# Kernel optimization log

Measured on AMD Instinct MI355X. Metric: run time of the kernel, lower is better.

The kernel has to match this reference:

```python
import jax, jax.numpy as jnp
import numpy as np

B, S, D = 2, 4096, 1024
H = 16            # num_attention_heads
HD = D // H       # head_dim = 64
WIN = 256         # sliding_window_size
STEP = WIN // 2   # loop stride in the original torch code
NB = S // STEP    # number of query blocks of size STEP
EPS = 1e-5


def setup_inputs() -> dict:
    key = jax.random.key(0)
    ks = jax.random.split(key, 6)
    lin = lambda k: jax.random.normal(k, (D, D), jnp.float32) * 0.02
    return {
        "hidden_states": jax.random.normal(ks[0], (B, S, D), jnp.float32),
        "Wq": lin(ks[1]), "bq": jnp.zeros((D,), jnp.float32),
        "Wk": lin(ks[2]), "bk": jnp.zeros((D,), jnp.float32),
        "Wv": lin(ks[3]), "bv": jnp.zeros((D,), jnp.float32),
        "Wo": lin(ks[4]), "bo": jnp.zeros((D,), jnp.float32),
        "ln_w": jnp.ones((D,), jnp.float32),
        "ln_b": jnp.zeros((D,), jnp.float32),
    }


def _split_heads(x):
    # [B,S,D] -> [B,H,S,HD]
    b, s, _ = x.shape
    return x.reshape(b, s, H, HD).transpose(0, 2, 1, 3)


def _forward(hidden_states, Wq, bq, Wk, bk, Wv, bv, Wo, bo, ln_w, ln_b):
    q = _split_heads(hidden_states @ Wq + bq)
    k = _split_heads(hidden_states @ Wk + bk)
    v = _split_heads(hidden_states @ Wv + bv)

    # windows overwrite earlier ones. Net effect: query block i (rows
    qb = q.reshape(B, H, NB, STEP, HD)
    kb = k.reshape(B, H, NB, STEP, HD)
    vb = v.reshape(B, H, NB, STEP, HD)
    zpad = jnp.zeros_like(kb[:, :, :1])
    k_win = jnp.concatenate([kb, jnp.concatenate([kb[:, :, 1:], zpad], axis=2)], axis=3)
    v_win = jnp.concatenate([vb, jnp.concatenate([vb[:, :, 1:], zpad], axis=2)], axis=3)

    scores = jnp.einsum("bhnqd,bhnkd->bhnqk", qb, k_win) / jnp.sqrt(jnp.float32(HD))
    # last block has only STEP valid keys (window truncated at seq end)
    blk = jnp.arange(NB)[:, None]
    kpos = jnp.arange(WIN)[None, :]
    valid = (blk < NB - 1) | (kpos < STEP)
    scores = jnp.where(valid[None, None, :, None, :], scores, -jnp.inf)
    attn = jax.nn.softmax(scores, axis=-1)
    outb = jnp.einsum("bhnqk,bhnkd->bhnqd", attn, v_win)  # [B,H,NB,STEP,HD]

    attn_out = outb.reshape(B, H, S, HD).transpose(0, 2, 1, 3).reshape(B, S, D)
    attn_out = attn_out @ Wo + bo

    x = hidden_states + attn_out
    mu = jnp.mean(x, axis=-1, keepdims=True)
    var = jnp.mean(jnp.square(x - mu), axis=-1, keepdims=True)
    return (x - mu) * jax.lax.rsqrt(var + EPS) * ln_w + ln_b


def reference(hidden_states, Wq, bq, Wk, bk, Wv, bv, Wo, bo, ln_w, ln_b):
    return _forward(hidden_states, Wq, bq, Wk, bk, Wv, bv, Wo, bo, ln_w, ln_b)
```

## Files before the change

kernel.cpp:

```cpp
#include <hip/hip_runtime.h>
#include <hip/hip_bf16.h>
#include <stdint.h>

#define D_MODEL 1024
#define SEQ     4096
#define NHEADS  16
#define HEAD_DIM 64
#define NBLK    32
#define MROWS   8192

typedef unsigned short u16;
using bf16x8 = __attribute__((ext_vector_type(8))) short;
using f32x4  = __attribute__((ext_vector_type(4))) float;

__device__ __forceinline__ float b2f(u16 b) {
  union { unsigned int u; float f; } v; v.u = ((unsigned int)b) << 16; return v.f;
}
__device__ __forceinline__ u16 f2b(float f) {
  union { float f; unsigned int u; } v; v.f = f;
  return (u16)((v.u + 0x7FFFu + ((v.u >> 16) & 1u)) >> 16);
}

__device__ __forceinline__ void gload16(const u16* g, u16* l) {
  __builtin_amdgcn_global_load_lds((const __attribute__((address_space(1))) void*)g,
                                   (__attribute__((address_space(3))) void*)l, 16, 0, 0);
}

__global__ __launch_bounds__(256) void convert_x_kernel(const float* __restrict__ X,
                                                        u16* __restrict__ Xb) {
  size_t idx = (size_t)blockIdx.x * 2048 + (size_t)threadIdx.x * 8;
  float4 a = *(const float4*)(X + idx);
  float4 b = *(const float4*)(X + idx + 4);
  union { u16 u[8]; uint4 v; } o;
  o.u[0]=f2b(a.x); o.u[1]=f2b(a.y); o.u[2]=f2b(a.z); o.u[3]=f2b(a.w);
  o.u[4]=f2b(b.x); o.u[5]=f2b(b.y); o.u[6]=f2b(b.z); o.u[7]=f2b(b.w);
  *(uint4*)(Xb + idx) = o.v;
}

__global__ __launch_bounds__(256) void transpose_w_kernel(const float* __restrict__ Wq,
                                                          const float* __restrict__ Wk,
                                                          const float* __restrict__ Wv,
                                                          const float* __restrict__ Wo,
                                                          u16* __restrict__ Wt) {
  const float* W = (blockIdx.z == 0) ? Wq : (blockIdx.z == 1) ? Wk
                 : (blockIdx.z == 2) ? Wv : Wo;
  u16* out = Wt + (size_t)blockIdx.z * D_MODEL * D_MODEL;
  __shared__ float t[32][33];
  int x = blockIdx.x * 32;
  int y = blockIdx.y * 32;
  int tx = threadIdx.x & 31, ty = threadIdx.x >> 5;
#pragma unroll
  for (int p = 0; p < 4; ++p)
    t[ty + p * 8][tx] = W[(size_t)(y + ty + p * 8) * D_MODEL + x + tx];
  __syncthreads();
#pragma unroll
  for (int p = 0; p < 4; ++p)
    out[(size_t)(x + ty + p * 8) * D_MODEL + y + tx] = f2b(t[tx][ty + p * 8]);
}

__device__ __forceinline__ void gemm_core(const u16* __restrict__ Ag,
                                          const u16* __restrict__ Bg,
                                          int m0, int n0,
                                          u16* smem, f32x4 acc[4][4]) {
  const int tid  = threadIdx.x;
  const int lane = tid & 63;
  const int w    = tid >> 6;
  const int wm   = w >> 1, wn = w & 1;
  const int fr   = lane & 15;

#pragma unroll
  for (int mf = 0; mf < 4; ++mf)
#pragma unroll
    for (int nf = 0; nf < 4; ++nf)
      acc[mf][nf] = (f32x4)(0.0f);

  const int srow = w * 32 + (lane >> 3);
  const int scol = (lane & 7) * 8;
  const u16* agp = Ag + (size_t)(m0 + srow) * D_MODEL + scol;
  const u16* bgp = Bg + (size_t)(n0 + srow) * D_MODEL + scol;
  u16* asl = smem + w * 2048;
  u16* bsl = smem + 8192 + w * 2048;

  const u16* ars = smem + (wm * 64 + fr) * 64 + (lane >> 4) * 8;
  const u16* brs = smem + 8192 + (wn * 64 + fr) * 64 + (lane >> 4) * 8;

  for (int kt = 0; kt < D_MODEL / 64; ++kt) {
#pragma unroll
    for (int j = 0; j < 4; ++j) {
      gload16(agp + (size_t)(j * 8) * D_MODEL, asl + j * 512);
      gload16(bgp + (size_t)(j * 8) * D_MODEL, bsl + j * 512);
    }
    agp += 64; bgp += 64;
    __syncthreads();
#pragma unroll
    for (int kk = 0; kk < 2; ++kk) {
      bf16x8 a[4], b[4];
#pragma unroll
      for (int mf = 0; mf < 4; ++mf)
        a[mf] = *(const bf16x8*)(ars + mf * 1024 + kk * 32);
#pragma unroll
      for (int nf = 0; nf < 4; ++nf)
        b[nf] = *(const bf16x8*)(brs + nf * 1024 + kk * 32);
#pragma unroll
      for (int mf = 0; mf < 4; ++mf)
#pragma unroll
        for (int nf = 0; nf < 4; ++nf)
          acc[mf][nf] = __builtin_amdgcn_mfma_f32_16x16x32_bf16(a[mf], b[nf],
                                                                acc[mf][nf], 0, 0, 0);
    }
    __syncthreads();
  }
}

__global__ __launch_bounds__(256, 2) void qkv_gemm_kernel(const u16* __restrict__ Xb,
                                                          const u16* __restrict__ Wt,
                                                          const float* __restrict__ bq,
                                                          const float* __restrict__ bk,
                                                          const float* __restrict__ bv,
                                                          u16* __restrict__ Qb,
                                                          u16* __restrict__ Kb,
                                                          u16* __restrict__ Vt) {
  __shared__ u16 smem[16384];
  const int id  = blockIdx.x;
  const int lin = (id & 7) * 192 + (id >> 3);
  const int which = lin % 3;
  const int nr  = lin / 3;
  const int n0  = (nr & 7) * 128;
  const int m0  = (nr >> 3) * 128;
  const u16* Bg = Wt + (size_t)which * D_MODEL * D_MODEL;
  f32x4 acc[4][4];
  gemm_core(Xb, Bg, m0, n0, smem, acc);

  const float* bias = (which == 0) ? bq : (which == 1) ? bk : bv;
  const float scale = (which == 0) ? 0.125f : 1.0f;
  const int lane = threadIdx.x & 63, w = threadIdx.x >> 6;
  const int wm = w >> 1, wn = w & 1;
  const int fr = lane & 15, fg = lane >> 4;
  const int mb = wm * 64 + fg * 4;
  const int nb = wn * 64 + fr;

  if (which < 2) {
#pragma unroll
    for (int nf = 0; nf < 4; ++nf) {
      const int n = nb + nf * 16;
      const float bn = bias[n0 + n];
#pragma unroll
      for (int mf = 0; mf < 4; ++mf)
#pragma unroll
        for (int r = 0; r < 4; ++r)
          smem[(mb + mf * 16 + r) * 128 + n] = f2b((acc[mf][nf][r] + bn) * scale);
    }
  } else {
#pragma unroll
    for (int nf = 0; nf < 4; ++nf) {
      const int n = nb + nf * 16;
      const float bn = bias[n0 + n];
#pragma unroll
      for (int mf = 0; mf < 4; ++mf)
#pragma unroll
        for (int r = 0; r < 4; ++r)
          smem[n * 128 + mb + mf * 16 + r] = f2b(acc[mf][nf][r] + bn);
    }
  }
  __syncthreads();

  u16* outQK = (which == 0) ? Qb : Kb;
#pragma unroll
  for (int it = 0; it < 2; ++it) {
    const int c   = threadIdx.x + it * 256;
    const int row = c >> 2;
    const int o32 = (c & 3) * 32;
    const u16* src = smem + row * 128 + o32;
    uint4 v0 = *(const uint4*)(src);
    uint4 v1 = *(const uint4*)(src + 8);
    uint4 v2 = *(const uint4*)(src + 16);
    uint4 v3 = *(const uint4*)(src + 24);
    u16* dst;
    if (which < 2) {
      const int mg = m0 + row;
      const int bb = mg >> 12, s = mg & 4095;
      const int n  = n0 + o32;
      const int h  = n >> 6, d0 = n & 63;
      dst = outQK + ((size_t)(bb * NHEADS + h) * SEQ + s) * HEAD_DIM + d0;
    } else {
      const int n  = n0 + row;
      const int h  = n >> 6, d = n & 63;
      const int bb = m0 >> 12;
      dst = Vt + ((size_t)(bb * NHEADS + h) * HEAD_DIM + d) * SEQ + (m0 & 4095) + o32;
    }
    *(uint4*)dst = v0; *(uint4*)(dst + 8) = v1;
    *(uint4*)(dst + 16) = v2; *(uint4*)(dst + 24) = v3;
  }
}

__global__ __launch_bounds__(256, 2) void o_gemm_kernel(const u16* __restrict__ X2,
                                                        const u16* __restrict__ WtO,
                                                        const float* __restrict__ bo,
                                                        u16* __restrict__ Y) {
  __shared__ u16 smem[16384];
  const int id  = blockIdx.x;
  const int lin = (id & 7) * 64 + (id >> 3);
  const int n0  = (lin & 7) * 128;
  const int m0  = (lin >> 3) * 128;
  f32x4 acc[4][4];
  gemm_core(X2, WtO, m0, n0, smem, acc);

  const int lane = threadIdx.x & 63, w = threadIdx.x >> 6;
  const int wm = w >> 1, wn = w & 1;
  const int fr = lane & 15, fg = lane >> 4;
  const int mb = wm * 64 + fg * 4;
  const int nb = wn * 64 + fr;
#pragma unroll
  for (int nf = 0; nf < 4; ++nf) {
    const int n = nb + nf * 16;
    const float bn = bo[n0 + n];
#pragma unroll
    for (int mf = 0; mf < 4; ++mf)
#pragma unroll
      for (int r = 0; r < 4; ++r)
        smem[(mb + mf * 16 + r) * 128 + n] = f2b(acc[mf][nf][r] + bn);
  }
  __syncthreads();
#pragma unroll
  for (int it = 0; it < 2; ++it) {
    const int c   = threadIdx.x + it * 256;
    const int row = c >> 2;
    const int o32 = (c & 3) * 32;
    const u16* src = smem + row * 128 + o32;
    uint4 v0 = *(const uint4*)(src);
    uint4 v1 = *(const uint4*)(src + 8);
    uint4 v2 = *(const uint4*)(src + 16);
    uint4 v3 = *(const uint4*)(src + 24);
    u16* dst = Y + (size_t)(m0 + row) * D_MODEL + n0 + o32;
    *(uint4*)dst = v0; *(uint4*)(dst + 8) = v1;
    *(uint4*)(dst + 16) = v2; *(uint4*)(dst + 24) = v3;
  }
}

#define PSTR 264
#define OSTR 72

template <int NF>
__device__ __forceinline__ void attn_body(const u16* __restrict__ Qp,
                                          const u16* __restrict__ Kp,
                                          const u16* __restrict__ Vp,
                                          u16* __restrict__ X2p,
                                          u16* Ps, float* rs) {
  const int lane = threadIdx.x & 63;
  const int fr = lane & 15, fg = lane >> 4;

  bf16x8 qf[2][2];
#pragma unroll
  for (int mf = 0; mf < 2; ++mf)
#pragma unroll
    for (int kk = 0; kk < 2; ++kk)
      qf[mf][kk] = *(const bf16x8*)(Qp + (mf * 16 + fr) * HEAD_DIM + kk * 32 + fg * 8);

  f32x4 sacc[2][NF];
#pragma unroll
  for (int mf = 0; mf < 2; ++mf)
#pragma unroll
    for (int nf = 0; nf < NF; ++nf) sacc[mf][nf] = (f32x4)(0.0f);

#pragma unroll
  for (int nf = 0; nf < NF; ++nf) {
    bf16x8 kf0 = *(const bf16x8*)(Kp + (nf * 16 + fr) * HEAD_DIM + fg * 8);
    bf16x8 kf1 = *(const bf16x8*)(Kp + (nf * 16 + fr) * HEAD_DIM + 32 + fg * 8);
#pragma unroll
    for (int mf = 0; mf < 2; ++mf) {
      sacc[mf][nf] = __builtin_amdgcn_mfma_f32_16x16x32_bf16(qf[mf][0], kf0, sacc[mf][nf], 0, 0, 0);
      sacc[mf][nf] = __builtin_amdgcn_mfma_f32_16x16x32_bf16(qf[mf][1], kf1, sacc[mf][nf], 0, 0, 0);
    }
  }

#pragma unroll
  for (int mf = 0; mf < 2; ++mf) {
#pragma unroll
    for (int r = 0; r < 4; ++r) {
      float mx = -1e30f;
#pragma unroll
      for (int nf = 0; nf < NF; ++nf) mx = fmaxf(mx, sacc[mf][nf][r]);
      mx = fmaxf(mx, __shfl_xor(mx, 1));
      mx = fmaxf(mx, __shfl_xor(mx, 2));
      mx = fmaxf(mx, __shfl_xor(mx, 4));
      mx = fmaxf(mx, __shfl_xor(mx, 8));
      float sm = 0.f;
#pragma unroll
      for (int nf = 0; nf < NF; ++nf) {
        float p = __expf(sacc[mf][nf][r] - mx);
        sacc[mf][nf][r] = p;
        sm += p;
      }
      sm += __shfl_xor(sm, 1);
      sm += __shfl_xor(sm, 2);
      sm += __shfl_xor(sm, 4);
      sm += __shfl_xor(sm, 8);
      if (fr == 0) rs[mf * 16 + fg * 4 + r] = sm;
    }
  }

#pragma unroll
  for (int mf = 0; mf < 2; ++mf)
#pragma unroll
    for (int nf = 0; nf < NF; ++nf)
#pragma unroll
      for (int r = 0; r < 4; ++r)
        Ps[(mf * 16 + fg * 4 + r) * PSTR + nf * 16 + fr] = f2b(sacc[mf][nf][r]);
  __syncthreads();

  f32x4 oacc[4][2];
#pragma unroll
  for (int mf2 = 0; mf2 < 4; ++mf2)
#pragma unroll
    for (int nf2 = 0; nf2 < 2; ++nf2) oacc[mf2][nf2] = (f32x4)(0.0f);

#pragma unroll
  for (int ks = 0; ks < NF / 2; ++ks) {
    bf16x8 vf[4];
#pragma unroll
    for (int mf2 = 0; mf2 < 4; ++mf2)
      vf[mf2] = *(const bf16x8*)(Vp + (size_t)(mf2 * 16 + fr) * SEQ + ks * 32 + fg * 8);
#pragma unroll
    for (int nf2 = 0; nf2 < 2; ++nf2) {
      bf16x8 pf = *(const bf16x8*)(Ps + (nf2 * 16 + fr) * PSTR + ks * 32 + fg * 8);
#pragma unroll
      for (int mf2 = 0; mf2 < 4; ++mf2)
        oacc[mf2][nf2] = __builtin_amdgcn_mfma_f32_16x16x32_bf16(vf[mf2], pf,
                                                                 oacc[mf2][nf2], 0, 0, 0);
    }
  }
  __syncthreads();

#pragma unroll
  for (int nf2 = 0; nf2 < 2; ++nf2) {
    const int q = nf2 * 16 + fr;
    const float inv = 1.0f / rs[q];
#pragma unroll
    for (int mf2 = 0; mf2 < 4; ++mf2)
#pragma unroll
      for (int r = 0; r < 4; ++r)
        Ps[q * OSTR + mf2 * 16 + fg * 4 + r] = f2b(oacc[mf2][nf2][r] * inv);
  }
  __syncthreads();
  const int q2 = lane >> 1, hf = (lane & 1) * 32;
  const u16* osrc = Ps + q2 * OSTR + hf;
  uint4 o0 = *(const uint4*)(osrc);
  uint4 o1 = *(const uint4*)(osrc + 8);
  uint4 o2 = *(const uint4*)(osrc + 16);
  uint4 o3 = *(const uint4*)(osrc + 24);
  u16* dst = X2p + (size_t)q2 * D_MODEL + hf;
  *(uint4*)dst = o0; *(uint4*)(dst + 8) = o1;
  *(uint4*)(dst + 16) = o2; *(uint4*)(dst + 24) = o3;
}

__global__ __launch_bounds__(256, 2) void attn_kernel(const u16* __restrict__ Qb,
                                                      const u16* __restrict__ Kb,
                                                      const u16* __restrict__ Vt,
                                                      u16* __restrict__ X2) {
  __shared__ u16 Ps[4][32 * PSTR];
  __shared__ float rs[4][32];
  const int bx = blockIdx.x;
  const int bh = bx >> 5, i = bx & 31;
  const int w = threadIdx.x >> 6;
  const int b = bh >> 4, h = bh & 15;
  const u16* Qp = Qb + ((size_t)bh * SEQ + i * 128 + w * 32) * HEAD_DIM;
  const u16* Kp = Kb + ((size_t)bh * SEQ + i * 128) * HEAD_DIM;
  const u16* Vp = Vt + (size_t)bh * HEAD_DIM * SEQ + i * 128;
  u16* X2p = X2 + ((size_t)(b * SEQ) + i * 128 + w * 32) * D_MODEL + h * HEAD_DIM;
  if (i == NBLK - 1) attn_body<8>(Qp, Kp, Vp, X2p, Ps[w], rs[w]);
  else               attn_body<16>(Qp, Kp, Vp, X2p, Ps[w], rs[w]);
}

__global__ __launch_bounds__(256) void ln_kernel(const float* __restrict__ hidden,
                                                 const u16* __restrict__ Y,
                                                 const float* __restrict__ lw,
                                                 const float* __restrict__ lb,
                                                 float* __restrict__ out) {
  const int row = blockIdx.x;
  const int tid = threadIdx.x;
  const size_t base = (size_t)row * D_MODEL + tid * 4;
  float4 h = *(const float4*)(hidden + base);
  union { uint2 v; u16 u[4]; } y;
  y.v = *(const uint2*)(Y + base);
  float x0 = h.x + b2f(y.u[0]);
  float x1 = h.y + b2f(y.u[1]);
  float x2 = h.z + b2f(y.u[2]);
  float x3 = h.w + b2f(y.u[3]);
  float sum = x0 + x1 + x2 + x3;
  float sq  = x0 * x0 + x1 * x1 + x2 * x2 + x3 * x3;
#pragma unroll
  for (int off = 32; off >= 1; off >>= 1) {
    sum += __shfl_down(sum, off);
    sq  += __shfl_down(sq, off);
  }
  __shared__ float s1[4], s2[4];
  const int w = tid >> 6, lane = tid & 63;
  if (lane == 0) { s1[w] = sum; s2[w] = sq; }
  __syncthreads();
  const float ts = s1[0] + s1[1] + s1[2] + s1[3];
  const float tq = s2[0] + s2[1] + s2[2] + s2[3];
  const float mu = ts * (1.0f / 1024.0f);
  const float var = tq * (1.0f / 1024.0f) - mu * mu;
  const float rstd = rsqrtf(var + 1e-5f);
  float4 lwv = *(const float4*)(lw + tid * 4);
  float4 lbv = *(const float4*)(lb + tid * 4);
  float4 o;
  o.x = (x0 - mu) * rstd * lwv.x + lbv.x;
  o.y = (x1 - mu) * rstd * lwv.y + lbv.y;
  o.z = (x2 - mu) * rstd * lwv.z + lbv.z;
  o.w = (x3 - mu) * rstd * lwv.w + lbv.w;
  *(float4*)(out + base) = o;
}

extern "C" void kernel_launch(void* const* d_in, const int* in_sizes, int n_in,
                              void* d_out, int out_size, void* d_ws, size_t ws_size,
                              hipStream_t stream) {
  const float* hidden = (const float*)d_in[0];
  const float* Wq = (const float*)d_in[1];
  const float* bq = (const float*)d_in[2];
  const float* Wk = (const float*)d_in[3];
  const float* bk = (const float*)d_in[4];
  const float* Wv = (const float*)d_in[5];
  const float* bv = (const float*)d_in[6];
  const float* Wo = (const float*)d_in[7];
  const float* bo = (const float*)d_in[8];
  const float* lw = (const float*)d_in[9];
  const float* lb = (const float*)d_in[10];
  float* out = (float*)d_out;

  u16* Xb = (u16*)d_ws;
  u16* Wt = Xb + (size_t)MROWS * D_MODEL;
  u16* Qb = Wt + (size_t)4 * D_MODEL * D_MODEL;
  u16* Kb = Qb + (size_t)32 * SEQ * HEAD_DIM;
  u16* Vt = Kb + (size_t)32 * SEQ * HEAD_DIM;
  u16* X2 = Vt + (size_t)32 * SEQ * HEAD_DIM;
  u16* Y  = X2 + (size_t)MROWS * D_MODEL;

  convert_x_kernel<<<4096, 256, 0, stream>>>(hidden, Xb);
  transpose_w_kernel<<<dim3(32, 32, 4), 256, 0, stream>>>(Wq, Wk, Wv, Wo, Wt);
  qkv_gemm_kernel<<<1536, 256, 0, stream>>>(Xb, Wt, bq, bk, bv, Qb, Kb, Vt);
  attn_kernel<<<1024, 256, 0, stream>>>(Qb, Kb, Vt, X2);
  o_gemm_kernel<<<512, 256, 0, stream>>>(X2, Wt + (size_t)3 * D_MODEL * D_MODEL, bo, Y);
  ln_kernel<<<MROWS, 256, 0, stream>>>(hidden, Y, lw, lb, out);
}
```

Baseline: 268.3 us.

## Double-buffer GEMM LDS tiles with prefetch and XOR-swizzled layout

The shared GEMM core now keeps two LDS buffers and issues the global-to-LDS loads for the next K tile before computing on the current one, waiting with a partial vmcnt so load latency overlaps the MFMA work. It also XOR-swizzles the 16-byte chunk placement in LDS to reduce bank conflicts on fragment reads. LDS per block doubles to 64 KB, which may limit how many blocks fit per CU at the requested occupancy of 2.

New measurement: 258.1 us. 3.8% less time.

```diff
diff --git a/kernel.cpp b/kernel.cpp
--- a/kernel.cpp
+++ b/kernel.cpp
@@ -8,6 +8,7 @@
 #define HEAD_DIM 64
 #define NBLK    32
 #define MROWS   8192
+#define NKT     16
 
 typedef unsigned short u16;
 using bf16x8 = __attribute__((ext_vector_type(8))) short;
@@ -67,6 +68,7 @@
   const int w    = tid >> 6;
   const int wm   = w >> 1, wn = w & 1;
   const int fr   = lane & 15;
+  const int fg   = lane >> 4;
 
 #pragma unroll
   for (int mf = 0; mf < 4; ++mf)
@@ -74,41 +76,64 @@
     for (int nf = 0; nf < 4; ++nf)
       acc[mf][nf] = (f32x4)(0.0f);
 
-  const int srow = w * 32 + (lane >> 3);
-  const int scol = (lane & 7) * 8;
-  const u16* agp = Ag + (size_t)(m0 + srow) * D_MODEL + scol;
-  const u16* bgp = Bg + (size_t)(n0 + srow) * D_MODEL + scol;
-  u16* asl = smem + w * 2048;
-  u16* bsl = smem + 8192 + w * 2048;
-
-  const u16* ars = smem + (wm * 64 + fr) * 64 + (lane >> 4) * 8;
-  const u16* brs = smem + 8192 + (wn * 64 + fr) * 64 + (lane >> 4) * 8;
-
-  for (int kt = 0; kt < D_MODEL / 64; ++kt) {
+  const int srow   = lane >> 3;
+  const int schunk = (lane & 7) ^ srow;
+  const u16* agp = Ag + (size_t)(m0 + w * 32 + srow) * D_MODEL + schunk * 8;
+  const u16* bgp = Bg + (size_t)(n0 + w * 32 + srow) * D_MODEL + schunk * 8;
+
+  const int c0 = fg ^ (fr & 7);
+  const int c1 = (4 + fg) ^ (fr & 7);
+  const u16* ars = smem + (wm * 64 + fr) * 64;
+  const u16* brs = smem + 8192 + (wn * 64 + fr) * 64;
+
+  auto stage = [&](int kt, int buf) {
+    u16* a_ = smem + buf * 16384 + w * 2048;
+    u16* b_ = smem + buf * 16384 + 8192 + w * 2048;
 #pragma unroll
     for (int j = 0; j < 4; ++j) {
-      gload16(agp + (size_t)(j * 8) * D_MODEL, asl + j * 512);
-      gload16(bgp + (size_t)(j * 8) * D_MODEL, bsl + j * 512);
-    }
-    agp += 64; bgp += 64;
-    __syncthreads();
-#pragma unroll
-    for (int kk = 0; kk < 2; ++kk) {
-      bf16x8 a[4], b[4];
-#pragma unroll
-      for (int mf = 0; mf < 4; ++mf)
-        a[mf] = *(const bf16x8*)(ars + mf * 1024 + kk * 32);
+      gload16(agp + (size_t)kt * 64 + (size_t)(j * 8) * D_MODEL, a_ + j * 512);
+      gload16(bgp + (size_t)kt * 64 + (size_t)(j * 8) * D_MODEL, b_ + j * 512);
+    }
+  };
+
+  stage(0, 0);
+  for (int kt = 0; kt < NKT; ++kt) {
+    if (kt + 1 < NKT) {
+      stage(kt + 1, (kt + 1) & 1);
+      asm volatile("s_waitcnt vmcnt(8)" ::: "memory");
+    } else {
+      asm volatile("s_waitcnt vmcnt(0)" ::: "memory");
+    }
+    __builtin_amdgcn_sched_barrier(0);
+    __builtin_amdgcn_s_barrier();
+    __builtin_amdgcn_sched_barrier(0);
+    const int boff = (kt & 1) * 16384;
+    bf16x8 a0[4], a1[4], b0[4], b1[4];
+#pragma unroll
+    for (int mf = 0; mf < 4; ++mf) {
+      a0[mf] = *(const bf16x8*)(ars + boff + mf * 1024 + c0 * 8);
+      a1[mf] = *(const bf16x8*)(ars + boff + mf * 1024 + c1 * 8);
+    }
+#pragma unroll
+    for (int nf = 0; nf < 4; ++nf) {
+      b0[nf] = *(const bf16x8*)(brs + boff + nf * 1024 + c0 * 8);
+      b1[nf] = *(const bf16x8*)(brs + boff + nf * 1024 + c1 * 8);
+    }
+#pragma unroll
+    for (int mf = 0; mf < 4; ++mf)
 #pragma unroll
       for (int nf = 0; nf < 4; ++nf)
-        b[nf] = *(const bf16x8*)(brs + nf * 1024 + kk * 32);
-#pragma unroll
-      for (int mf = 0; mf < 4; ++mf)
-#pragma unroll
-        for (int nf = 0; nf < 4; ++nf)
-          acc[mf][nf] = __builtin_amdgcn_mfma_f32_16x16x32_bf16(a[mf], b[nf],
-                                                                acc[mf][nf], 0, 0, 0);
-    }
-    __syncthreads();
+        acc[mf][nf] = __builtin_amdgcn_mfma_f32_16x16x32_bf16(a0[mf], b0[nf],
+                                                              acc[mf][nf], 0, 0, 0);
+#pragma unroll
+    for (int mf = 0; mf < 4; ++mf)
+#pragma unroll
+      for (int nf = 0; nf < 4; ++nf)
+        acc[mf][nf] = __builtin_amdgcn_mfma_f32_16x16x32_bf16(a1[mf], b1[nf],
+                                                              acc[mf][nf], 0, 0, 0);
+    __builtin_amdgcn_sched_barrier(0);
+    __builtin_amdgcn_s_barrier();
+    __builtin_amdgcn_sched_barrier(0);
   }
 }
 
@@ -120,7 +145,7 @@
                                                           u16* __restrict__ Qb,
                                                           u16* __restrict__ Kb,
                                                           u16* __restrict__ Vt) {
-  __shared__ u16 smem[16384];
+  __shared__ u16 smem[32768];
   const int id  = blockIdx.x;
   const int lin = (id & 7) * 192 + (id >> 3);
   const int which = lin % 3;
@@ -197,7 +222,7 @@
                                                         const u16* __restrict__ WtO,
                                                         const float* __restrict__ bo,
                                                         u16* __restrict__ Y) {
-  __shared__ u16 smem[16384];
+  __shared__ u16 smem[32768];
   const int id  = blockIdx.x;
   const int lin = (id & 7) * 64 + (id >> 3);
   const int n0  = (lin & 7) * 128;
```

## Rewrite GEMM core as 256x256 tile, 8-wave double-buffered swizzled pipeline

Applied to the files above, without the earlier changes.

Replaces the 128x128 single-buffered GEMM core with a 256x256-tile core using 8 waves, double-buffered LDS with XOR-swizzled layout, and interleaved global-to-LDS prefetch of the next k-tile between MFMA phases. It adds explicit barriers, sched_barrier fences and setprio around the MFMA bursts. Both the QKV and output projection kernels use it with fewer, larger blocks. The goal is more data reuse per LDS byte, less bank conflict and hidden load latency. The cost is 128KB LDS per block and far fewer blocks: 384 for QKV and only 128 for the output GEMM, which may underfill the GPU's CUs.

Result: slower. 277.3 us (+3.3%).

```diff
diff --git a/kernel.cpp b/kernel.cpp
--- a/kernel.cpp
+++ b/kernel.cpp
@@ -8,6 +8,7 @@
 #define HEAD_DIM 64
 #define NBLK    32
 #define MROWS   8192
+#define NKT     16
 
 typedef unsigned short u16;
 using bf16x8 = __attribute__((ext_vector_type(8))) short;
@@ -25,6 +26,8 @@
   __builtin_amdgcn_global_load_lds((const __attribute__((address_space(1))) void*)g,
                                    (__attribute__((address_space(3))) void*)l, 16, 0, 0);
 }
+#define SCHED() __builtin_amdgcn_sched_barrier(0)
+#define BAR()   __builtin_amdgcn_s_barrier()
 
 __global__ __launch_bounds__(256) void convert_x_kernel(const float* __restrict__ X,
                                                         u16* __restrict__ Xb) {
@@ -58,61 +61,115 @@
     out[(size_t)(x + ty + p * 8) * D_MODEL + y + tx] = f2b(t[tx][ty + p * 8]);
 }
 
-__device__ __forceinline__ void gemm_core(const u16* __restrict__ Ag,
-                                          const u16* __restrict__ Bg,
-                                          int m0, int n0,
-                                          u16* smem, f32x4 acc[4][4]) {
+__device__ __forceinline__ void gemm_core8(const u16* __restrict__ Ag,
+                                           const u16* __restrict__ Bg,
+                                           int m0, int n0,
+                                           u16* smem, f32x4 acc[8][4]) {
   const int tid  = threadIdx.x;
   const int lane = tid & 63;
   const int w    = tid >> 6;
-  const int wm   = w >> 1, wn = w & 1;
-  const int fr   = lane & 15;
-
-#pragma unroll
-  for (int mf = 0; mf < 4; ++mf)
+  const int wm   = w >> 2, wn = w & 3;
+  const int fr   = lane & 15, fg = lane >> 4;
+
+#pragma unroll
+  for (int mf = 0; mf < 8; ++mf)
 #pragma unroll
     for (int nf = 0; nf < 4; ++nf)
       acc[mf][nf] = (f32x4)(0.0f);
 
-  const int srow = w * 32 + (lane >> 3);
-  const int scol = (lane & 7) * 8;
-  const u16* agp = Ag + (size_t)(m0 + srow) * D_MODEL + scol;
-  const u16* bgp = Bg + (size_t)(n0 + srow) * D_MODEL + scol;
-  u16* asl = smem + w * 2048;
-  u16* bsl = smem + 8192 + w * 2048;
-
-  const u16* ars = smem + (wm * 64 + fr) * 64 + (lane >> 4) * 8;
-  const u16* brs = smem + 8192 + (wn * 64 + fr) * 64 + (lane >> 4) * 8;
-
-  for (int kt = 0; kt < D_MODEL / 64; ++kt) {
-#pragma unroll
-    for (int j = 0; j < 4; ++j) {
-      gload16(agp + (size_t)(j * 8) * D_MODEL, asl + j * 512);
-      gload16(bgp + (size_t)(j * 8) * D_MODEL, bsl + j * 512);
-    }
-    agp += 64; bgp += 64;
-    __syncthreads();
-#pragma unroll
-    for (int kk = 0; kk < 2; ++kk) {
-      bf16x8 a[4], b[4];
-#pragma unroll
-      for (int mf = 0; mf < 4; ++mf)
-        a[mf] = *(const bf16x8*)(ars + mf * 1024 + kk * 32);
+  const int srow = lane >> 3;
+  const int schk = (lane & 7) ^ srow;
+  const u16* agp = Ag + (size_t)(m0 + w * 16 + srow) * D_MODEL + schk * 8;
+  const u16* bgp = Bg + (size_t)(n0 + w * 16 + srow) * D_MODEL + schk * 8;
+
+  const int arow = (wm * 128 + fr) * 64;
+  const int brow = 16384 + (wn * 64 + fr) * 64;
+  const int c0 = (fg ^ (fr & 7)) * 8;
+  const int c1 = ((4 + fg) ^ (fr & 7)) * 8;
+
+  auto stA = [&](int kt, int h) {
+    u16* dst = smem + (kt & 1) * 32768 + h * 8192 + w * 1024;
+    const u16* src = agp + (size_t)(h * 128) * D_MODEL + (size_t)kt * 64;
+    gload16(src, dst);
+    gload16(src + (size_t)8 * D_MODEL, dst + 512);
+  };
+  auto stB = [&](int kt, int h) {
+    u16* dst = smem + (kt & 1) * 32768 + 16384 + h * 8192 + w * 1024;
+    const u16* src = bgp + (size_t)(h * 128) * D_MODEL + (size_t)kt * 64;
+    gload16(src, dst);
+    gload16(src + (size_t)8 * D_MODEL, dst + 512);
+  };
+
+  stA(0, 0); stB(0, 0); stA(0, 1); stB(0, 1);
+  asm volatile("s_waitcnt vmcnt(0)" ::: "memory");
+  SCHED(); BAR(); SCHED();
+
+  bf16x8 a[4], bk0[4], bk1[4];
+  for (int t = 0; t < NKT; ++t) {
+    const int bo = (t & 1) * 32768;
+#pragma unroll
+    for (int i = 0; i < 4; ++i) a[i]   = *(const bf16x8*)(smem + bo + arow + i * 1024 + c0);
+#pragma unroll
+    for (int i = 0; i < 4; ++i) bk0[i] = *(const bf16x8*)(smem + bo + brow + i * 1024 + c0);
+    if (t + 1 < NKT) { stA(t + 1, 0); stB(t + 1, 0); }
+    SCHED(); BAR();
+    asm volatile("s_waitcnt lgkmcnt(0)" ::: "memory");
+    SCHED();
+    __builtin_amdgcn_s_setprio(1);
+#pragma unroll
+    for (int i = 0; i < 4; ++i)
 #pragma unroll
       for (int nf = 0; nf < 4; ++nf)
-        b[nf] = *(const bf16x8*)(brs + nf * 1024 + kk * 32);
-#pragma unroll
-      for (int mf = 0; mf < 4; ++mf)
-#pragma unroll
-        for (int nf = 0; nf < 4; ++nf)
-          acc[mf][nf] = __builtin_amdgcn_mfma_f32_16x16x32_bf16(a[mf], b[nf],
-                                                                acc[mf][nf], 0, 0, 0);
-    }
-    __syncthreads();
-  }
-}
-
-__global__ __launch_bounds__(256, 2) void qkv_gemm_kernel(const u16* __restrict__ Xb,
+        acc[i][nf] = __builtin_amdgcn_mfma_f32_16x16x32_bf16(a[i], bk0[nf], acc[i][nf], 0, 0, 0);
+    __builtin_amdgcn_s_setprio(0);
+    SCHED(); BAR(); SCHED();
+#pragma unroll
+    for (int i = 0; i < 4; ++i) a[i]   = *(const bf16x8*)(smem + bo + arow + i * 1024 + c1);
+#pragma unroll
+    for (int i = 0; i < 4; ++i) bk1[i] = *(const bf16x8*)(smem + bo + brow + i * 1024 + c1);
+    if (t + 1 < NKT) { stA(t + 1, 1); stB(t + 1, 1); }
+    SCHED(); BAR();
+    asm volatile("s_waitcnt lgkmcnt(0)" ::: "memory");
+    SCHED();
+    __builtin_amdgcn_s_setprio(1);
+#pragma unroll
+    for (int i = 0; i < 4; ++i)
+#pragma unroll
+      for (int nf = 0; nf < 4; ++nf)
+        acc[i][nf] = __builtin_amdgcn_mfma_f32_16x16x32_bf16(a[i], bk1[nf], acc[i][nf], 0, 0, 0);
+    __builtin_amdgcn_s_setprio(0);
+    SCHED(); BAR(); SCHED();
+#pragma unroll
+    for (int i = 0; i < 4; ++i) a[i] = *(const bf16x8*)(smem + bo + arow + (4 + i) * 1024 + c0);
+    SCHED(); BAR();
+    asm volatile("s_waitcnt lgkmcnt(0)" ::: "memory");
+    SCHED();
+    __builtin_amdgcn_s_setprio(1);
+#pragma unroll
+    for (int i = 0; i < 4; ++i)
+#pragma unroll
+      for (int nf = 0; nf < 4; ++nf)
+        acc[4 + i][nf] = __builtin_amdgcn_mfma_f32_16x16x32_bf16(a[i], bk0[nf], acc[4 + i][nf], 0, 0, 0);
+    __builtin_amdgcn_s_setprio(0);
+    SCHED(); BAR(); SCHED();
+#pragma unroll
+    for (int i = 0; i < 4; ++i) a[i] = *(const bf16x8*)(smem + bo + arow + (4 + i) * 1024 + c1);
+    asm volatile("s_waitcnt vmcnt(0)" ::: "memory");
+    SCHED(); BAR();
+    asm volatile("s_waitcnt lgkmcnt(0)" ::: "memory");
+    SCHED();
+    __builtin_amdgcn_s_setprio(1);
+#pragma unroll
+    for (int i = 0; i < 4; ++i)
+#pragma unroll
+      for (int nf = 0; nf < 4; ++nf)
+        acc[4 + i][nf] = __builtin_amdgcn_mfma_f32_16x16x32_bf16(a[i], bk1[nf], acc[4 + i][nf], 0, 0, 0);
+    __builtin_amdgcn_s_setprio(0);
+    SCHED(); BAR(); SCHED();
+  }
+}
+
+__global__ __launch_bounds__(512, 2) void qkv_gemm_kernel(const u16* __restrict__ Xb,
                                                           const u16* __restrict__ Wt,
                                                           const float* __restrict__ bq,
                                                           const float* __restrict__ bk,
@@ -120,57 +177,60 @@
                                                           u16* __restrict__ Qb,
                                                           u16* __restrict__ Kb,
                                                           u16* __restrict__ Vt) {
-  __shared__ u16 smem[16384];
+  __shared__ u16 smem[65536];
   const int id  = blockIdx.x;
-  const int lin = (id & 7) * 192 + (id >> 3);
-  const int which = lin % 3;
-  const int nr  = lin / 3;
-  const int n0  = (nr & 7) * 128;
-  const int m0  = (nr >> 3) * 128;
+  const int lin = (id & 7) * 48 + (id >> 3);
+  const int mt  = lin / 12;
+  const int rem = lin % 12;
+  const int nt  = rem / 3;
+  const int which = rem % 3;
+  const int m0 = mt * 256, n0 = nt * 256;
   const u16* Bg = Wt + (size_t)which * D_MODEL * D_MODEL;
-  f32x4 acc[4][4];
-  gemm_core(Xb, Bg, m0, n0, smem, acc);
+  f32x4 acc[8][4];
+  gemm_core8(Xb, Bg, m0, n0, smem, acc);
 
   const float* bias = (which == 0) ? bq : (which == 1) ? bk : bv;
   const float scale = (which == 0) ? 0.125f : 1.0f;
   const int lane = threadIdx.x & 63, w = threadIdx.x >> 6;
-  const int wm = w >> 1, wn = w & 1;
+  const int wm = w >> 2, wn = w & 3;
   const int fr = lane & 15, fg = lane >> 4;
-  const int mb = wm * 64 + fg * 4;
-  const int nb = wn * 64 + fr;
 
   if (which < 2) {
 #pragma unroll
     for (int nf = 0; nf < 4; ++nf) {
-      const int n = nb + nf * 16;
+      const int n = wn * 64 + nf * 16 + fr;
       const float bn = bias[n0 + n];
 #pragma unroll
-      for (int mf = 0; mf < 4; ++mf)
-#pragma unroll
-        for (int r = 0; r < 4; ++r)
-          smem[(mb + mf * 16 + r) * 128 + n] = f2b((acc[mf][nf][r] + bn) * scale);
+      for (int mf = 0; mf < 8; ++mf)
+#pragma unroll
+        for (int r = 0; r < 4; ++r) {
+          const int row = wm * 128 + mf * 16 + fg * 4 + r;
+          smem[row * 256 + n] = f2b((acc[mf][nf][r] + bn) * scale);
+        }
     }
   } else {
 #pragma unroll
     for (int nf = 0; nf < 4; ++nf) {
-      const int n = nb + nf * 16;
+      const int n = wn * 64 + nf * 16 + fr;
       const float bn = bias[n0 + n];
 #pragma unroll
-      for (int mf = 0; mf < 4; ++mf)
-#pragma unroll
-        for (int r = 0; r < 4; ++r)
-          smem[n * 128 + mb + mf * 16 + r] = f2b(acc[mf][nf][r] + bn);
+      for (int mf = 0; mf < 8; ++mf)
+#pragma unroll
+        for (int r = 0; r < 4; ++r) {
+          const int row = wm * 128 + mf * 16 + fg * 4 + r;
+          smem[n * 256 + row] = f2b(acc[mf][nf][r] + bn);
+        }
     }
   }
   __syncthreads();
 
   u16* outQK = (which == 0) ? Qb : Kb;
 #pragma unroll
-  for (int it = 0; it < 2; ++it) {
-    const int c   = threadIdx.x + it * 256;
-    const int row = c >> 2;
-    const int o32 = (c & 3) * 32;
-    const u16* src = smem + row * 128 + o32;
+  for (int it = 0; it < 4; ++it) {
+    const int c   = it * 512 + threadIdx.x;
+    const int row = c >> 3;
+    const int o32 = (c & 7) * 32;
+    const u16* src = smem + row * 256 + o32;
     uint4 v0 = *(const uint4*)(src);
     uint4 v1 = *(const uint4*)(src + 8);
     uint4 v2 = *(const uint4*)(src + 16);
@@ -179,12 +239,12 @@
     if (which < 2) {
       const int mg = m0 + row;
       const int bb = mg >> 12, s = mg & 4095;
-      const int n  = n0 + o32;
-      const int h  = n >> 6, d0 = n & 63;
+      const int nn = n0 + o32;
+      const int h  = nn >> 6, d0 = nn & 63;
       dst = outQK + ((size_t)(bb * NHEADS + h) * SEQ + s) * HEAD_DIM + d0;
     } else {
-      const int n  = n0 + row;
-      const int h  = n >> 6, d = n & 63;
+      const int nn = n0 + row;
+      const int h  = nn >> 6, d = nn & 63;
       const int bb = m0 >> 12;
       dst = Vt + ((size_t)(bb * NHEADS + h) * HEAD_DIM + d) * SEQ + (m0 & 4095) + o32;
     }
@@ -193,40 +253,40 @@
   }
 }
 
-__global__ __launch_bounds__(256, 2) void o_gemm_kernel(const u16* __restrict__ X2,
+__global__ __launch_bounds__(512, 2) void o_gemm_kernel(const u16* __restrict__ X2,
                                                         const u16* __restrict__ WtO,
                                                         const float* __restrict__ bo,
                                                         u16* __restrict__ Y) {
-  __shared__ u16 smem[16384];
+  __shared__ u16 smem[65536];
   const int id  = blockIdx.x;
-  const int lin = (id & 7) * 64 + (id >> 3);
-  const int n0  = (lin & 7) * 128;
-  const int m0  = (lin >> 3) * 128;
-  f32x4 acc[4][4];
-  gemm_core(X2, WtO, m0, n0, smem, acc);
+  const int lin = (id & 7) * 16 + (id >> 3);
+  const int m0  = (lin >> 2) * 256;
+  const int n0  = (lin & 3) * 256;
+  f32x4 acc[8][4];
+  gemm_core8(X2, WtO, m0, n0, smem, acc);
 
   const int lane = threadIdx.x & 63, w = threadIdx.x >> 6;
-  const int wm = w >> 1, wn = w & 1;
+  const int wm = w >> 2, wn = w & 3;
   const int fr = lane & 15, fg = lane >> 4;
-  const int mb = wm * 64 + fg * 4;
-  const int nb = wn * 64 + fr;
 #pragma unroll
   for (int nf = 0; nf < 4; ++nf) {
-    const int n = nb + nf * 16;
+    const int n = wn * 64 + nf * 16 + fr;
     const float bn = bo[n0 + n];
 #pragma unroll
-    for (int mf = 0; mf < 4; ++mf)
-#pragma unroll
-      for (int r = 0; r < 4; ++r)
-        smem[(mb + mf * 16 + r) * 128 + n] = f2b(acc[mf][nf][r] + bn);
-  }
-  __syncthreads();
-#pragma unroll
-  for (int it = 0; it < 2; ++it) {
-    const int c   = threadIdx.x + it * 256;
-    const int row = c >> 2;
-    const int o32 = (c & 3) * 32;
-    const u16* src = smem + row * 128 + o32;
+    for (int mf = 0; mf < 8; ++mf)
+#pragma unroll
+      for (int r = 0; r < 4; ++r) {
+        const int row = wm * 128 + mf * 16 + fg * 4 + r;
+        smem[row * 256 + n] = f2b(acc[mf][nf][r] + bn);
+      }
+  }
+  __syncthreads();
+#pragma unroll
+  for (int it = 0; it < 4; ++it) {
+    const int c   = it * 512 + threadIdx.x;
+    const int row = c >> 3;
+    const int o32 = (c & 7) * 32;
+    const u16* src = smem + row * 256 + o32;
     uint4 v0 = *(const uint4*)(src);
     uint4 v1 = *(const uint4*)(src + 8);
     uint4 v2 = *(const uint4*)(src + 16);
@@ -438,8 +498,8 @@
 
   convert_x_kernel<<<4096, 256, 0, stream>>>(hidden, Xb);
   transpose_w_kernel<<<dim3(32, 32, 4), 256, 0, stream>>>(Wq, Wk, Wv, Wo, Wt);
-  qkv_gemm_kernel<<<1536, 256, 0, stream>>>(Xb, Wt, bq, bk, bv, Qb, Kb, Vt);
+  qkv_gemm_kernel<<<384, 512, 0, stream>>>(Xb, Wt, bq, bk, bv, Qb, Kb, Vt);
   attn_kernel<<<1024, 256, 0, stream>>>(Qb, Kb, Vt, X2);
-  o_gemm_kernel<<<512, 256, 0, stream>>>(X2, Wt + (size_t)3 * D_MODEL * D_MODEL, bo, Y);
+  o_gemm_kernel<<<128, 512, 0, stream>>>(X2, Wt + (size_t)3 * D_MODEL * D_MODEL, bo, Y);
   ln_kernel<<<MROWS, 256, 0, stream>>>(hidden, Y, lw, lb, out);
 }
```
